# Kernel optimization log

Hardware: AMD Instinct MI355X
Metric: run time of the kernel (lower is better)

The kernel has to match this reference:

```python
import jax, jax.numpy as jnp
import numpy as np

N, T, D_IN, D_OUT = 131072, 16, 128, 128


def setup_inputs() -> dict:
    key = jax.random.key(0)
    k1, k2, k3, k4 = jax.random.split(key, 4)
    x = jax.random.normal(k1, (N, D_IN), dtype=jnp.float32)
    # sorted type ids, matching HeteroLinear(is_sorted=True)
    type_vec = jnp.sort(jax.random.randint(k2, (N,), 0, T)).astype(jnp.int32)
    # HeteroLinear weight: [num_types, in_channels, out_channels]; out = x @ W[t] + b[t]
    weight = (jax.random.normal(k3, (T, D_IN, D_OUT), dtype=jnp.float32)
              / np.float32(np.sqrt(D_IN)))
    bias = jax.random.normal(k4, (T, D_OUT), dtype=jnp.float32) * 0.01
    return {"x": x, "type_vec": type_vec, "weight": weight, "bias": bias}


def _grouped_matmul(x, weight, type_vec):
    """Segment (grouped) matmul: rows are sorted by type; row i uses weight[type_vec[i]]."""
    try:
        # Native grouped-GEMM primitive (exploits is_sorted=True contiguity).
        group_sizes = jnp.bincount(type_vec, length=weight.shape[0]).astype(jnp.int32)
        return jax.lax.ragged_dot(x, weight, group_sizes)
    except Exception:
        # Fallback: small fixed loop over the T types, masked accumulate.
        out = jnp.zeros((x.shape[0], weight.shape[-1]), dtype=x.dtype)
        for t in range(weight.shape[0]):
            out = out + jnp.where((type_vec == t)[:, None], x @ weight[t], jnp.zeros((), x.dtype))
        return out


def reference(x, type_vec, weight, bias):
    # ToHeteroLinear.fused_forward == HeteroLinear(x, type_vec):
    #   out[i] = x[i] @ weight[type_vec[i]] + bias[type_vec[i]]
    out = _grouped_matmul(x, weight, type_vec)  # [N, D_OUT]
    return out + bias[type_vec]
```

## Files before the change

kernel.cpp:

```cpp
#include <hip/hip_runtime.h>

#define DD 128
#define BM 64
#define CHUNK 2
#define T_TYPES 16

typedef __bf16 bf16x8 __attribute__((ext_vector_type(8)));
typedef float  f32x4  __attribute__((ext_vector_type(4)));

__device__ __forceinline__ void build_B(const float* __restrict__ wt,
                                        __bf16* __restrict__ Bs, int tid) {
    #pragma unroll
    for (int i = 0; i < 8; ++i) {
        int F    = tid + (i << 8);
        int lane = F & 63;
        int kk   = (F >> 6) & 3;
        int nt   = F >> 8;
        int q    = lane >> 4;
        int n16  = lane & 15;
        const float* p = wt + (kk * 32 + q * 8) * DD + nt * 16 + n16;
        bf16x8 v;
        #pragma unroll
        for (int j = 0; j < 8; ++j) v[j] = (__bf16)p[j * DD];
        *(bf16x8*)&Bs[(size_t)F * 8] = v;
    }
}

__global__ __launch_bounds__(256, 4) void hetero_fused_kernel(
    const float* __restrict__ x,
    const int*   __restrict__ tv,
    const float* __restrict__ w,
    const float* __restrict__ bias,
    float*       __restrict__ out)
{
    __shared__ __bf16 Bs[DD * DD];

    const int tid  = threadIdx.x;
    const int wave = tid >> 6;
    const int lane = tid & 63;
    const int q    = lane >> 4;
    const int n16  = lane & 15;
    const int chunk0 = blockIdx.x * (BM * CHUNK);

    int t_res = tv[chunk0];

    f32x4 xlo[4], xhi[4];
    {
        const float* base = x + (size_t)(chunk0 + wave * 16 + n16) * DD + q * 8;
        #pragma unroll
        for (int kk = 0; kk < 4; ++kk) {
            xlo[kk] = *(const f32x4*)(base + kk * 32);
            xhi[kk] = *(const f32x4*)(base + kk * 32 + 4);
        }
    }

    build_B(w + (size_t)t_res * DD * DD, Bs, tid);

    float bv[8];
    #pragma unroll
    for (int nt = 0; nt < 8; ++nt) bv[nt] = bias[t_res * DD + nt * 16 + n16];

    __syncthreads();

    #pragma unroll
    for (int tile = 0; tile < CHUNK; ++tile) {
        const int trow0 = chunk0 + tile * BM;
        const int wrow0 = trow0 + wave * 16;

        f32x4 nlo[4], nhi[4];
        if (tile + 1 < CHUNK) {
            const float* base = x + (size_t)(wrow0 + BM + n16) * DD + q * 8;
            #pragma unroll
            for (int kk = 0; kk < 4; ++kk) {
                nlo[kk] = *(const f32x4*)(base + kk * 32);
                nhi[kk] = *(const f32x4*)(base + kk * 32 + 4);
            }
        }

        bf16x8 a[4];
        #pragma unroll
        for (int kk = 0; kk < 4; ++kk) {
            bf16x8 t;
            t[0] = (__bf16)xlo[kk][0]; t[1] = (__bf16)xlo[kk][1];
            t[2] = (__bf16)xlo[kk][2]; t[3] = (__bf16)xlo[kk][3];
            t[4] = (__bf16)xhi[kk][0]; t[5] = (__bf16)xhi[kk][1];
            t[6] = (__bf16)xhi[kk][2]; t[7] = (__bf16)xhi[kk][3];
            a[kk] = t;
        }

        const int tlo = tv[trow0];
        const int thi = tv[trow0 + BM - 1];

        for (int t = tlo; t <= thi; ++t) {
            if (t != t_res) {
                __syncthreads();
                build_B(w + (size_t)t * DD * DD, Bs, tid);
                t_res = t;
                #pragma unroll
                for (int nt = 0; nt < 8; ++nt) bv[nt] = bias[t * DD + nt * 16 + n16];
                __syncthreads();
            }

            f32x4 acc[8];
            #pragma unroll
            for (int nt = 0; nt < 8; ++nt) acc[nt] = (f32x4){0.f, 0.f, 0.f, 0.f};

            #pragma unroll
            for (int nt = 0; nt < 8; ++nt) {
                #pragma unroll
                for (int kk = 0; kk < 4; ++kk) {
                    bf16x8 b = *(const bf16x8*)&Bs[(((nt << 2) | kk) << 9) | (lane << 3)];
                    acc[nt] = __builtin_amdgcn_mfma_f32_16x16x32_bf16(a[kk], b, acc[nt], 0, 0, 0);
                }
            }

            const int rbase = wrow0 + q * 4;
            bool m0 = true, m1 = true, m2 = true, m3 = true;
            if (tlo != thi) {
                m0 = (tv[rbase + 0] == t);
                m1 = (tv[rbase + 1] == t);
                m2 = (tv[rbase + 2] == t);
                m3 = (tv[rbase + 3] == t);
            }
            float* o = out + (size_t)rbase * DD + n16;
            #pragma unroll
            for (int nt = 0; nt < 8; ++nt) {
                float* oc = o + nt * 16;
                if (m0) oc[0 * DD] = acc[nt][0] + bv[nt];
                if (m1) oc[1 * DD] = acc[nt][1] + bv[nt];
                if (m2) oc[2 * DD] = acc[nt][2] + bv[nt];
                if (m3) oc[3 * DD] = acc[nt][3] + bv[nt];
            }
        }

        #pragma unroll
        for (int kk = 0; kk < 4; ++kk) { xlo[kk] = nlo[kk]; xhi[kk] = nhi[kk]; }
    }
}

extern "C" void kernel_launch(void* const* d_in, const int* in_sizes, int n_in,
                              void* d_out, int out_size, void* d_ws, size_t ws_size,
                              hipStream_t stream) {
    const float* x    = (const float*)d_in[0];
    const int*   tv   = (const int*)d_in[1];
    const float* w    = (const float*)d_in[2];
    const float* bias = (const float*)d_in[3];
    float*       out  = (float*)d_out;

    int nrows = in_sizes[0] / DD;
    int grid  = nrows / (BM * CHUNK);

    hipLaunchKernelGGL(hetero_fused_kernel, dim3(grid), dim3(256), 0, stream,
                       x, tv, w, bias, out);
}
```

Baseline: 127.2 us.

## Hold per-type weights in registers per wave instead of shared LDS tile

```diff
diff --git a/kernel.cpp b/kernel.cpp
--- a/kernel.cpp
+++ b/kernel.cpp
@@ -1,81 +1,61 @@
 #include <hip/hip_runtime.h>
 
 #define DD 128
-#define BM 64
-#define CHUNK 2
-#define T_TYPES 16
+#define TILES 4
 
 typedef __bf16 bf16x8 __attribute__((ext_vector_type(8)));
 typedef float  f32x4  __attribute__((ext_vector_type(4)));
 
-__device__ __forceinline__ void build_B(const float* __restrict__ wt,
-                                        __bf16* __restrict__ Bs, int tid) {
+__device__ __forceinline__ void gather_W(const float* __restrict__ wt,
+                                         int q, int n16,
+                                         bf16x8 wf[8][4]) {
     #pragma unroll
-    for (int i = 0; i < 8; ++i) {
-        int F    = tid + (i << 8);
-        int lane = F & 63;
-        int kk   = (F >> 6) & 3;
-        int nt   = F >> 8;
-        int q    = lane >> 4;
-        int n16  = lane & 15;
-        const float* p = wt + (kk * 32 + q * 8) * DD + nt * 16 + n16;
-        bf16x8 v;
+    for (int nt = 0; nt < 8; ++nt) {
         #pragma unroll
-        for (int j = 0; j < 8; ++j) v[j] = (__bf16)p[j * DD];
-        *(bf16x8*)&Bs[(size_t)F * 8] = v;
+        for (int kk = 0; kk < 4; ++kk) {
+            const float* p = wt + (kk * 32 + q * 8) * DD + nt * 16 + n16;
+            bf16x8 v;
+            #pragma unroll
+            for (int j = 0; j < 8; ++j) v[j] = (__bf16)p[j * DD];
+            wf[nt][kk] = v;
+        }
     }
 }
 
-__global__ __launch_bounds__(256, 4) void hetero_fused_kernel(
+__global__ __launch_bounds__(64, 2) void hetero_reg_kernel(
     const float* __restrict__ x,
     const int*   __restrict__ tv,
     const float* __restrict__ w,
     const float* __restrict__ bias,
     float*       __restrict__ out)
 {
-    __shared__ __bf16 Bs[DD * DD];
-
-    const int tid  = threadIdx.x;
-    const int wave = tid >> 6;
-    const int lane = tid & 63;
+    const int lane = threadIdx.x;
     const int q    = lane >> 4;
     const int n16  = lane & 15;
-    const int chunk0 = blockIdx.x * (BM * CHUNK);
-
-    int t_res = tv[chunk0];
+    const int row_base = blockIdx.x * (16 * TILES);
 
     f32x4 xlo[4], xhi[4];
     {
-        const float* base = x + (size_t)(chunk0 + wave * 16 + n16) * DD + q * 8;
+        const float* b0 = x + (size_t)(row_base + n16) * DD + q * 8;
         #pragma unroll
         for (int kk = 0; kk < 4; ++kk) {
-            xlo[kk] = *(const f32x4*)(base + kk * 32);
-            xhi[kk] = *(const f32x4*)(base + kk * 32 + 4);
+            xlo[kk] = *(const f32x4*)(b0 + kk * 32);
+            xhi[kk] = *(const f32x4*)(b0 + kk * 32 + 4);
         }
     }
 
-    build_B(w + (size_t)t_res * DD * DD, Bs, tid);
+    int t_res = tv[row_base];
+
+    bf16x8 wf[8][4];
+    gather_W(w + (size_t)t_res * DD * DD, q, n16, wf);
 
     float bv[8];
     #pragma unroll
     for (int nt = 0; nt < 8; ++nt) bv[nt] = bias[t_res * DD + nt * 16 + n16];
 
-    __syncthreads();
-
     #pragma unroll
-    for (int tile = 0; tile < CHUNK; ++tile) {
-        const int trow0 = chunk0 + tile * BM;
-        const int wrow0 = trow0 + wave * 16;
-
-        f32x4 nlo[4], nhi[4];
-        if (tile + 1 < CHUNK) {
-            const float* base = x + (size_t)(wrow0 + BM + n16) * DD + q * 8;
-            #pragma unroll
-            for (int kk = 0; kk < 4; ++kk) {
-                nlo[kk] = *(const f32x4*)(base + kk * 32);
-                nhi[kk] = *(const f32x4*)(base + kk * 32 + 4);
-            }
-        }
+    for (int tile = 0; tile < TILES; ++tile) {
+        const int row0 = row_base + tile * 16;
 
         bf16x8 a[4];
         #pragma unroll
@@ -88,17 +68,24 @@
             a[kk] = t;
         }
 
-        const int tlo = tv[trow0];
-        const int thi = tv[trow0 + BM - 1];
+        if (tile + 1 < TILES) {
+            const float* bn = x + (size_t)(row0 + 16 + n16) * DD + q * 8;
+            #pragma unroll
+            for (int kk = 0; kk < 4; ++kk) {
+                xlo[kk] = *(const f32x4*)(bn + kk * 32);
+                xhi[kk] = *(const f32x4*)(bn + kk * 32 + 4);
+            }
+        }
+
+        const int tlo = tv[row0];
+        const int thi = tv[row0 + 15];
 
         for (int t = tlo; t <= thi; ++t) {
             if (t != t_res) {
-                __syncthreads();
-                build_B(w + (size_t)t * DD * DD, Bs, tid);
-                t_res = t;
+                gather_W(w + (size_t)t * DD * DD, q, n16, wf);
                 #pragma unroll
                 for (int nt = 0; nt < 8; ++nt) bv[nt] = bias[t * DD + nt * 16 + n16];
-                __syncthreads();
+                t_res = t;
             }
 
             f32x4 acc[8];
@@ -108,13 +95,12 @@
             #pragma unroll
             for (int nt = 0; nt < 8; ++nt) {
                 #pragma unroll
-                for (int kk = 0; kk < 4; ++kk) {
-                    bf16x8 b = *(const bf16x8*)&Bs[(((nt << 2) | kk) << 9) | (lane << 3)];
-                    acc[nt] = __builtin_amdgcn_mfma_f32_16x16x32_bf16(a[kk], b, acc[nt], 0, 0, 0);
-                }
+                for (int kk = 0; kk < 4; ++kk)
+                    acc[nt] = __builtin_amdgcn_mfma_f32_16x16x32_bf16(
+                        a[kk], wf[nt][kk], acc[nt], 0, 0, 0);
             }
 
-            const int rbase = wrow0 + q * 4;
+            const int rbase = row0 + q * 4;
             bool m0 = true, m1 = true, m2 = true, m3 = true;
             if (tlo != thi) {
                 m0 = (tv[rbase + 0] == t);
@@ -132,9 +118,6 @@
                 if (m3) oc[3 * DD] = acc[nt][3] + bv[nt];
             }
         }
-
-        #pragma unroll
-        for (int kk = 0; kk < 4; ++kk) { xlo[kk] = nlo[kk]; xhi[kk] = nhi[kk]; }
     }
 }
 
@@ -148,8 +131,8 @@
     float*       out  = (float*)d_out;
 
     int nrows = in_sizes[0] / DD;
-    int grid  = nrows / (BM * CHUNK);
+    int grid  = nrows / (16 * TILES);
 
-    hipLaunchKernelGGL(hetero_fused_kernel, dim3(grid), dim3(256), 0, stream,
+    hipLaunchKernelGGL(hetero_reg_kernel, dim3(grid), dim3(64), 0, stream,
                        x, tv, w, bias, out);
 }
```

New measurement: 135.4 us. 1.06x slower.
